# Optimization experiments

Measured on AMD Instinct MI355X. Metric: run time of the kernel, lower is better.

## Reference

```python
import jax, jax.numpy as jnp
import numpy as np

EMB = 768
HEADS = 12
HEAD_DIM = EMB // HEADS  # 64
SCALE = HEAD_DIM ** -0.5


def setup_inputs() -> dict:
    key = jax.random.key(0)
    ks = jax.random.split(key, 9)
    B, S = 32, 576
    s = EMB ** -0.5
    return {
        "hidden_states": jax.random.normal(ks[0], (B, S, EMB), jnp.float32),
        "q_w": jax.random.normal(ks[1], (EMB, EMB), jnp.float32) * s,
        "q_b": jnp.zeros((EMB,), jnp.float32),
        "k_w": jax.random.normal(ks[2], (EMB, EMB), jnp.float32) * s,
        "k_b": jnp.zeros((EMB,), jnp.float32),
        "v_w": jax.random.normal(ks[3], (EMB, EMB), jnp.float32) * s,
        "v_b": jnp.zeros((EMB,), jnp.float32),
        "o_w": jax.random.normal(ks[4], (EMB, EMB), jnp.float32) * s,
        "o_b": jnp.zeros((EMB,), jnp.float32),
    }


def reference(hidden_states, q_w, q_b, k_w, k_b, v_w, v_b, o_w, o_b):
    B, S, _ = hidden_states.shape
    # Linear projections (torch Linear: x @ W^T + b)
    q = hidden_states @ q_w.T + q_b
    k = hidden_states @ k_w.T + k_b
    v = hidden_states @ v_w.T + v_b
    # [B, H, S, D]
    q = q.reshape(B, S, HEADS, HEAD_DIM).transpose(0, 2, 1, 3)
    k = k.reshape(B, S, HEADS, HEAD_DIM).transpose(0, 2, 1, 3)
    v = v.reshape(B, S, HEADS, HEAD_DIM).transpose(0, 2, 1, 3)
    # Full N x N attention scores, softmax in fp32 (as in source)
    scores = jnp.einsum('bhqd,bhkd->bhqk', q, k) * SCALE
    attn = jax.nn.softmax(scores.astype(jnp.float32), axis=-1).astype(q.dtype)
    # dropout p=0.0 -> identity
    out = jnp.einsum('bhqk,bhkd->bhqd', attn, v)  # [B, H, S, D]
    out = out.transpose(0, 2, 1, 3).reshape(B, S, EMB)
    out = out @ o_w.T + o_b
    return (out, attn)
```

## Files before the change

### kernel.cpp

```cpp
#include <hip/hip_runtime.h>


#define B_ 32
#define S_ 576
#define H_ 12
#define D_ 64
#define E_ 768
#define M_ (B_ * S_)

typedef __attribute__((ext_vector_type(8))) short bf16x8;
typedef __attribute__((ext_vector_type(4))) float f32x4;
typedef __attribute__((ext_vector_type(4))) unsigned short u16x4;
typedef __attribute__((ext_vector_type(8))) unsigned short u16x8;

#define MFMA16(a, b, c) __builtin_amdgcn_mfma_f32_16x16x32_bf16(a, b, c, 0, 0, 0)

__device__ __forceinline__ unsigned short f2bf(float x) {
  union { float f; unsigned u; } v; v.f = x;
  unsigned r = v.u + 0x7fffu + ((v.u >> 16) & 1u);
  return (unsigned short)(r >> 16);
}
__device__ __forceinline__ float bf2f(unsigned short h) {
  union { unsigned u; float f; } v; v.u = ((unsigned)h) << 16; return v.f;
}

__global__ __launch_bounds__(256) void cvt_split(const float* __restrict__ in,
                                                 unsigned short* __restrict__ hi,
                                                 unsigned short* __restrict__ lo,
                                                 int n4) {
  int i = blockIdx.x * 256 + threadIdx.x;
  if (i >= n4) return;
  float4 x = ((const float4*)in)[i];
  u16x4 h;
  h[0] = f2bf(x.x); h[1] = f2bf(x.y); h[2] = f2bf(x.z); h[3] = f2bf(x.w);
  ((u16x4*)hi)[i] = h;
  if (lo) {
    u16x4 l;
    l[0] = f2bf(x.x - bf2f(h[0])); l[1] = f2bf(x.y - bf2f(h[1]));
    l[2] = f2bf(x.z - bf2f(h[2])); l[3] = f2bf(x.w - bf2f(h[3]));
    ((u16x4*)lo)[i] = l;
  }
}

template <bool SPLIT, int OUT_MODE>
__global__ __launch_bounds__(256)
void gemm128(const unsigned short* __restrict__ Ahg, const unsigned short* __restrict__ Alg,
             const unsigned short* __restrict__ Bhg, const unsigned short* __restrict__ Blg,
             const float* __restrict__ bias, void* __restrict__ C0, void* __restrict__ C1,
             int Kd, int lda, int ldb, int ldc) {
  constexpr int BM = 128, BN = 128, BK = 32, LSTR = BK + 8;
  __shared__ __attribute__((aligned(16))) unsigned short Ah[BM * LSTR];
  __shared__ __attribute__((aligned(16))) unsigned short Bh[BN * LSTR];
  __shared__ __attribute__((aligned(16))) unsigned short Al[SPLIT ? BM * LSTR : 8];
  __shared__ __attribute__((aligned(16))) unsigned short Bl[SPLIT ? BN * LSTR : 8];

  const int tid = threadIdx.x, lane = tid & 63, wv = tid >> 6;
  const int wm = (wv & 1) * 64, wn = (wv >> 1) * 64;
  const long m0 = (long)blockIdx.y * BM, n0 = (long)blockIdx.x * BN;
  const int fr = lane & 15, g8 = (lane >> 4) * 8;

  f32x4 acc[4][4] = {};

  for (int kt = 0; kt < Kd; kt += BK) {
    __syncthreads();
    for (int i = tid; i < BM * BK / 8; i += 256) {
      int row = i >> 2, c8 = (i & 3) * 8;
      *(u16x8*)&Ah[row * LSTR + c8] = *(const u16x8*)(Ahg + (m0 + row) * lda + kt + c8);
      *(u16x8*)&Bh[row * LSTR + c8] = *(const u16x8*)(Bhg + (n0 + row) * ldb + kt + c8);
      if (SPLIT) {
        *(u16x8*)&Al[row * LSTR + c8] = *(const u16x8*)(Alg + (m0 + row) * lda + kt + c8);
        *(u16x8*)&Bl[row * LSTR + c8] = *(const u16x8*)(Blg + (n0 + row) * ldb + kt + c8);
      }
    }
    __syncthreads();
    bf16x8 ah[4], bh[4], al[4], bl[4];
#pragma unroll
    for (int mi = 0; mi < 4; ++mi) {
      ah[mi] = *(const bf16x8*)&Ah[(wm + mi * 16 + fr) * LSTR + g8];
      if (SPLIT) al[mi] = *(const bf16x8*)&Al[(wm + mi * 16 + fr) * LSTR + g8];
    }
#pragma unroll
    for (int ni = 0; ni < 4; ++ni) {
      bh[ni] = *(const bf16x8*)&Bh[(wn + ni * 16 + fr) * LSTR + g8];
      if (SPLIT) bl[ni] = *(const bf16x8*)&Bl[(wn + ni * 16 + fr) * LSTR + g8];
    }
#pragma unroll
    for (int mi = 0; mi < 4; ++mi)
#pragma unroll
      for (int ni = 0; ni < 4; ++ni) {
        acc[mi][ni] = MFMA16(ah[mi], bh[ni], acc[mi][ni]);
        if (SPLIT) {
          acc[mi][ni] = MFMA16(ah[mi], bl[ni], acc[mi][ni]);
          acc[mi][ni] = MFMA16(al[mi], bh[ni], acc[mi][ni]);
        }
      }
  }

#pragma unroll
  for (int mi = 0; mi < 4; ++mi)
#pragma unroll
    for (int ni = 0; ni < 4; ++ni) {
      long col = n0 + wn + ni * 16 + fr;
      long rb = m0 + wm + mi * 16 + (lane >> 4) * 4;
      float bv = bias ? bias[col] : 0.f;
#pragma unroll
      for (int r = 0; r < 4; ++r) {
        float v = acc[mi][ni][r] + bv;
        long idx = (rb + r) * ldc + col;
        if (OUT_MODE == 0) {
          ((float*)C0)[idx] = v;
        } else if (OUT_MODE == 1) {
          ((unsigned short*)C0)[idx] = f2bf(v);
        } else {
          unsigned short hh = f2bf(v);
          ((unsigned short*)C0)[idx] = hh;
          ((unsigned short*)C1)[idx] = f2bf(v - bf2f(hh));
        }
      }
    }
}

__global__ __launch_bounds__(256)
void attn_softmax(const unsigned short* __restrict__ qh, const unsigned short* __restrict__ ql,
                  const unsigned short* __restrict__ kh, const unsigned short* __restrict__ kl,
                  float* __restrict__ attn) {
  constexpr int LQ = 72;
  __shared__ __attribute__((aligned(16))) unsigned short qhl[32 * LQ], qll[32 * LQ];
  __shared__ __attribute__((aligned(16))) unsigned short khl[64 * LQ], kll[64 * LQ];
  __shared__ float redm[2][32], reds[2][32];

  const int tid = threadIdx.x, lane = tid & 63, wv = tid >> 6;
  const int qt = blockIdx.x, h = blockIdx.y, b = blockIdx.z;
  const int fr = lane & 15, gq = lane >> 4;
  const int mg = (wv & 1), ch = (wv >> 1);

  {
    int row = tid >> 3, c8 = (tid & 7) * 8;
    long qb = ((long)(b * S_ + qt * 32 + row)) * E_ + h * 64 + c8;
    *(u16x8*)&qhl[row * LQ + c8] = *(const u16x8*)(qh + qb);
    *(u16x8*)&qll[row * LQ + c8] = *(const u16x8*)(ql + qb);
  }
  __syncthreads();
  bf16x8 qa_h[2], qa_l[2];
#pragma unroll
  for (int kc = 0; kc < 2; ++kc) {
    qa_h[kc] = *(const bf16x8*)&qhl[(mg * 16 + fr) * LQ + kc * 32 + gq * 8];
    qa_l[kc] = *(const bf16x8*)&qll[(mg * 16 + fr) * LQ + kc * 32 + gq * 8];
  }

  f32x4 acc[9][2] = {};
  for (int kt = 0; kt < 9; ++kt) {
    __syncthreads();
    for (int i = tid; i < 512; i += 256) {
      int row = i >> 3, c8 = (i & 7) * 8;
      long kb = ((long)(b * S_ + kt * 64 + row)) * E_ + h * 64 + c8;
      *(u16x8*)&khl[row * LQ + c8] = *(const u16x8*)(kh + kb);
      *(u16x8*)&kll[row * LQ + c8] = *(const u16x8*)(kl + kb);
    }
    __syncthreads();
#pragma unroll
    for (int kc = 0; kc < 2; ++kc) {
#pragma unroll
      for (int nf = 0; nf < 2; ++nf) {
        bf16x8 b_h = *(const bf16x8*)&khl[(ch * 32 + nf * 16 + fr) * LQ + kc * 32 + gq * 8];
        bf16x8 b_l = *(const bf16x8*)&kll[(ch * 32 + nf * 16 + fr) * LQ + kc * 32 + gq * 8];
        acc[kt][nf] = MFMA16(qa_h[kc], b_h, acc[kt][nf]);
        acc[kt][nf] = MFMA16(qa_h[kc], b_l, acc[kt][nf]);
        acc[kt][nf] = MFMA16(qa_l[kc], b_h, acc[kt][nf]);
      }
    }
  }

  const float SC = 0.125f;
  float M[4], Sv[4];
#pragma unroll
  for (int r = 0; r < 4; ++r) {
    float pm = -1e30f;
#pragma unroll
    for (int kt = 0; kt < 9; ++kt)
#pragma unroll
      for (int nf = 0; nf < 2; ++nf) pm = fmaxf(pm, acc[kt][nf][r] * SC);
    for (int off = 1; off < 16; off <<= 1) pm = fmaxf(pm, __shfl_xor(pm, off));
    M[r] = pm;
  }
  if (fr == 0) {
#pragma unroll
    for (int r = 0; r < 4; ++r) redm[ch][mg * 16 + gq * 4 + r] = M[r];
  }
  __syncthreads();
#pragma unroll
  for (int r = 0; r < 4; ++r)
    M[r] = fmaxf(redm[0][mg * 16 + gq * 4 + r], redm[1][mg * 16 + gq * 4 + r]);

#pragma unroll
  for (int r = 0; r < 4; ++r) {
    float ps = 0.f;
#pragma unroll
    for (int kt = 0; kt < 9; ++kt)
#pragma unroll
      for (int nf = 0; nf < 2; ++nf) {
        float e = __expf(acc[kt][nf][r] * SC - M[r]);
        acc[kt][nf][r] = e;
        ps += e;
      }
    for (int off = 1; off < 16; off <<= 1) ps += __shfl_xor(ps, off);
    Sv[r] = ps;
  }
  if (fr == 0) {
#pragma unroll
    for (int r = 0; r < 4; ++r) reds[ch][mg * 16 + gq * 4 + r] = Sv[r];
  }
  __syncthreads();
#pragma unroll
  for (int r = 0; r < 4; ++r)
    Sv[r] = 1.f / (reds[0][mg * 16 + gq * 4 + r] + reds[1][mg * 16 + gq * 4 + r]);

  float* out = attn + ((long)((b * H_ + h) * S_) + qt * 32) * S_;
#pragma unroll
  for (int kt = 0; kt < 9; ++kt)
#pragma unroll
    for (int nf = 0; nf < 2; ++nf)
#pragma unroll
      for (int r = 0; r < 4; ++r) {
        long row = mg * 16 + gq * 4 + r;
        long col = kt * 64 + ch * 32 + nf * 16 + fr;
        out[row * S_ + col] = acc[kt][nf][r] * Sv[r];
      }
}

__global__ __launch_bounds__(256)
void pv_kernel(const float* __restrict__ attn, const unsigned short* __restrict__ v,
               unsigned short* __restrict__ out_pre) {
  constexpr int LSTR = 40;
  __shared__ __attribute__((aligned(16))) unsigned short A_lds[64 * LSTR];
  __shared__ __attribute__((aligned(16))) unsigned short B_lds[64 * LSTR];

  const int tid = threadIdx.x, lane = tid & 63, wv = tid >> 6;
  const int mt = blockIdx.x, z = blockIdx.y;
  const int b = z / 12, h = z % 12;
  const int wm = (wv & 1) * 32, wn = (wv >> 1) * 32;
  const int fr = lane & 15, g8 = (lane >> 4) * 8;

  const float* Ab = attn + (long)z * S_ * S_ + (long)mt * 64 * S_;
  const unsigned short* Vb = v + (long)b * S_ * E_ + h * 64;

  f32x4 acc[2][2] = {};
  for (int kt = 0; kt < S_; kt += 32) {
    __syncthreads();
    for (int i = tid; i < 512; i += 256) {
      int row = i >> 3, c4 = (i & 7) * 4;
      float4 x = *(const float4*)(Ab + (long)row * S_ + kt + c4);
      u16x4 hh;
      hh[0] = f2bf(x.x); hh[1] = f2bf(x.y); hh[2] = f2bf(x.z); hh[3] = f2bf(x.w);
      *(u16x4*)&A_lds[row * LSTR + c4] = hh;
    }
    for (int i = tid; i < 512; i += 256) {
      int kk = i >> 4, d4 = (i & 15) * 4;
      u16x4 x = *(const u16x4*)(Vb + (long)(kt + kk) * E_ + d4);
#pragma unroll
      for (int j = 0; j < 4; ++j) B_lds[(d4 + j) * LSTR + kk] = x[j];
    }
    __syncthreads();
    bf16x8 af[2], bfv[2];
#pragma unroll
    for (int mi = 0; mi < 2; ++mi) af[mi] = *(const bf16x8*)&A_lds[(wm + mi * 16 + fr) * LSTR + g8];
#pragma unroll
    for (int ni = 0; ni < 2; ++ni) bfv[ni] = *(const bf16x8*)&B_lds[(wn + ni * 16 + fr) * LSTR + g8];
#pragma unroll
    for (int mi = 0; mi < 2; ++mi)
#pragma unroll
      for (int ni = 0; ni < 2; ++ni) acc[mi][ni] = MFMA16(af[mi], bfv[ni], acc[mi][ni]);
  }

#pragma unroll
  for (int mi = 0; mi < 2; ++mi)
#pragma unroll
    for (int ni = 0; ni < 2; ++ni)
#pragma unroll
      for (int r = 0; r < 4; ++r) {
        long row = (long)mt * 64 + wm + mi * 16 + (lane >> 4) * 4 + r;
        long col = wn + ni * 16 + fr;
        out_pre[((long)b * S_ + row) * E_ + h * 64 + col] = f2bf(acc[mi][ni][r]);
      }
}

extern "C" void kernel_launch(void* const* d_in, const int* in_sizes, int n_in,
                              void* d_out, int out_size, void* d_ws, size_t ws_size,
                              hipStream_t stream) {
  const float* X = (const float*)d_in[0];
  const float* q_w = (const float*)d_in[1];
  const float* q_b = (const float*)d_in[2];
  const float* k_w = (const float*)d_in[3];
  const float* k_b = (const float*)d_in[4];
  const float* v_w = (const float*)d_in[5];
  const float* v_b = (const float*)d_in[6];
  const float* o_w = (const float*)d_in[7];
  const float* o_b = (const float*)d_in[8];

  const long NX = (long)M_ * E_;
  const long NW = (long)E_ * E_;

  unsigned short* w = (unsigned short*)d_ws;
  unsigned short* Xhi = w;
  unsigned short* Xlo = Xhi + NX;
  unsigned short* qwh = Xlo + NX;
  unsigned short* qwl = qwh + NW;
  unsigned short* kwh = qwl + NW;
  unsigned short* kwl = kwh + NW;
  unsigned short* vwh = kwl + NW;
  unsigned short* owh = vwh + NW;
  unsigned short* Qhi = owh + NW;
  unsigned short* Qlo = Qhi + NX;
  unsigned short* Khi = Qlo + NX;
  unsigned short* Klo = Khi + NX;
  unsigned short* Vw  = Klo + NX;
  unsigned short* Opre = Vw + NX;

  float* out_f = (float*)d_out;
  float* attn_f = (float*)d_out + NX;

  cvt_split<<<dim3((NX / 4 + 255) / 256), dim3(256), 0, stream>>>(X, Xhi, Xlo, NX / 4);
  cvt_split<<<dim3((NW / 4 + 255) / 256), dim3(256), 0, stream>>>(q_w, qwh, qwl, NW / 4);
  cvt_split<<<dim3((NW / 4 + 255) / 256), dim3(256), 0, stream>>>(k_w, kwh, kwl, NW / 4);
  cvt_split<<<dim3((NW / 4 + 255) / 256), dim3(256), 0, stream>>>(v_w, vwh, nullptr, NW / 4);
  cvt_split<<<dim3((NW / 4 + 255) / 256), dim3(256), 0, stream>>>(o_w, owh, nullptr, NW / 4);

  dim3 gproj(E_ / 128, M_ / 128);
  gemm128<true, 2><<<gproj, dim3(256), 0, stream>>>(Xhi, Xlo, qwh, qwl, q_b, Qhi, Qlo, E_, E_, E_, E_);
  gemm128<true, 2><<<gproj, dim3(256), 0, stream>>>(Xhi, Xlo, kwh, kwl, k_b, Khi, Klo, E_, E_, E_, E_);
  gemm128<false, 1><<<gproj, dim3(256), 0, stream>>>(Xhi, nullptr, vwh, nullptr, v_b, Vw, nullptr, E_, E_, E_, E_);

  attn_softmax<<<dim3(S_ / 32, H_, B_), dim3(256), 0, stream>>>(Qhi, Qlo, Khi, Klo, attn_f);

  pv_kernel<<<dim3(S_ / 64, B_ * H_), dim3(256), 0, stream>>>(attn_f, Vw, Opre);

  gemm128<false, 0><<<gproj, dim3(256), 0, stream>>>(Opre, nullptr, owh, nullptr, o_b, out_f, nullptr, E_, E_, E_, E_);
}
```

Measured before the change: 1.216 ms.

## Fuse PV matmul into attention-softmax kernel with transposed V layout

Merges the separate PV kernel into the softmax kernel. The normalized probabilities are kept as bf16 in LDS and multiplied by V directly, so the fp32 attention matrix no longer has to be re-read from global memory. The V projection GEMM now writes V transposed per head ([B,H,D,S]) so V tiles load contiguously, and the attention output uses nontemporal stores. This adds a large P buffer in LDS (about 37KB), which may reduce occupancy, and the transposed V write is a strided scatter.

Measured after the change: 1.197 ms. No clear change (-1.6%).

```diff
diff --git a/kernel.cpp b/kernel.cpp
--- a/kernel.cpp
+++ b/kernel.cpp
@@ -111,23 +111,33 @@
           ((float*)C0)[idx] = v;
         } else if (OUT_MODE == 1) {
           ((unsigned short*)C0)[idx] = f2bf(v);
-        } else {
+        } else if (OUT_MODE == 2) {
           unsigned short hh = f2bf(v);
           ((unsigned short*)C0)[idx] = hh;
           ((unsigned short*)C1)[idx] = f2bf(v - bf2f(hh));
+        } else {
+          long m = rb + r;
+          int bb = (int)(m / S_);
+          int ss = (int)(m - (long)bb * S_);
+          int hh2 = (int)(col >> 6), dd = (int)(col & 63);
+          ((unsigned short*)C0)[(((long)bb * H_ + hh2) * D_ + dd) * S_ + ss] = f2bf(v);
         }
       }
     }
 }
 
 __global__ __launch_bounds__(256)
-void attn_softmax(const unsigned short* __restrict__ qh, const unsigned short* __restrict__ ql,
-                  const unsigned short* __restrict__ kh, const unsigned short* __restrict__ kl,
-                  float* __restrict__ attn) {
+void attn_pv(const unsigned short* __restrict__ qh, const unsigned short* __restrict__ ql,
+             const unsigned short* __restrict__ kh, const unsigned short* __restrict__ kl,
+             const unsigned short* __restrict__ vt,
+             float* __restrict__ attn, unsigned short* __restrict__ out_pre) {
   constexpr int LQ = 72;
+  constexpr int LP = 584;
   __shared__ __attribute__((aligned(16))) unsigned short qhl[32 * LQ], qll[32 * LQ];
   __shared__ __attribute__((aligned(16))) unsigned short khl[64 * LQ], kll[64 * LQ];
+  __shared__ __attribute__((aligned(16))) unsigned short P_lds[32 * LP];
   __shared__ float redm[2][32], reds[2][32];
+  unsigned short* Vt = kll;
 
   const int tid = threadIdx.x, lane = tid & 63, wv = tid >> 6;
   const int qt = blockIdx.x, h = blockIdx.y, b = blockIdx.z;
@@ -222,66 +232,41 @@
     for (int nf = 0; nf < 2; ++nf)
 #pragma unroll
       for (int r = 0; r < 4; ++r) {
-        long row = mg * 16 + gq * 4 + r;
-        long col = kt * 64 + ch * 32 + nf * 16 + fr;
-        out[row * S_ + col] = acc[kt][nf][r] * Sv[r];
-      }
-}
-
-__global__ __launch_bounds__(256)
-void pv_kernel(const float* __restrict__ attn, const unsigned short* __restrict__ v,
-               unsigned short* __restrict__ out_pre) {
-  constexpr int LSTR = 40;
-  __shared__ __attribute__((aligned(16))) unsigned short A_lds[64 * LSTR];
-  __shared__ __attribute__((aligned(16))) unsigned short B_lds[64 * LSTR];
-
-  const int tid = threadIdx.x, lane = tid & 63, wv = tid >> 6;
-  const int mt = blockIdx.x, z = blockIdx.y;
-  const int b = z / 12, h = z % 12;
-  const int wm = (wv & 1) * 32, wn = (wv >> 1) * 32;
-  const int fr = lane & 15, g8 = (lane >> 4) * 8;
-
-  const float* Ab = attn + (long)z * S_ * S_ + (long)mt * 64 * S_;
-  const unsigned short* Vb = v + (long)b * S_ * E_ + h * 64;
-
-  f32x4 acc[2][2] = {};
-  for (int kt = 0; kt < S_; kt += 32) {
+        int row = mg * 16 + gq * 4 + r;
+        int col = kt * 64 + ch * 32 + nf * 16 + fr;
+        float val = acc[kt][nf][r] * Sv[r];
+        __builtin_nontemporal_store(val, &out[(long)row * S_ + col]);
+        P_lds[row * LP + col] = f2bf(val);
+      }
+
+  const unsigned short* Vb = vt + ((long)(b * H_ + h)) * D_ * S_;
+  f32x4 accp[2] = {};
+  for (int kt2 = 0; kt2 < 9; ++kt2) {
     __syncthreads();
     for (int i = tid; i < 512; i += 256) {
-      int row = i >> 3, c4 = (i & 7) * 4;
-      float4 x = *(const float4*)(Ab + (long)row * S_ + kt + c4);
-      u16x4 hh;
-      hh[0] = f2bf(x.x); hh[1] = f2bf(x.y); hh[2] = f2bf(x.z); hh[3] = f2bf(x.w);
-      *(u16x4*)&A_lds[row * LSTR + c4] = hh;
-    }
-    for (int i = tid; i < 512; i += 256) {
-      int kk = i >> 4, d4 = (i & 15) * 4;
-      u16x4 x = *(const u16x4*)(Vb + (long)(kt + kk) * E_ + d4);
-#pragma unroll
-      for (int j = 0; j < 4; ++j) B_lds[(d4 + j) * LSTR + kk] = x[j];
-    }
-    __syncthreads();
-    bf16x8 af[2], bfv[2];
-#pragma unroll
-    for (int mi = 0; mi < 2; ++mi) af[mi] = *(const bf16x8*)&A_lds[(wm + mi * 16 + fr) * LSTR + g8];
-#pragma unroll
-    for (int ni = 0; ni < 2; ++ni) bfv[ni] = *(const bf16x8*)&B_lds[(wn + ni * 16 + fr) * LSTR + g8];
-#pragma unroll
-    for (int mi = 0; mi < 2; ++mi)
-#pragma unroll
-      for (int ni = 0; ni < 2; ++ni) acc[mi][ni] = MFMA16(af[mi], bfv[ni], acc[mi][ni]);
-  }
-
-#pragma unroll
-  for (int mi = 0; mi < 2; ++mi)
-#pragma unroll
-    for (int ni = 0; ni < 2; ++ni)
-#pragma unroll
-      for (int r = 0; r < 4; ++r) {
-        long row = (long)mt * 64 + wm + mi * 16 + (lane >> 4) * 4 + r;
-        long col = wn + ni * 16 + fr;
-        out_pre[((long)b * S_ + row) * E_ + h * 64 + col] = f2bf(acc[mi][ni][r]);
-      }
+      int row = i >> 3, c8 = (i & 7) * 8;
+      *(u16x8*)&Vt[row * LQ + c8] = *(const u16x8*)(Vb + (long)row * S_ + kt2 * 64 + c8);
+    }
+    __syncthreads();
+#pragma unroll
+    for (int kc = 0; kc < 2; ++kc) {
+      bf16x8 a = *(const bf16x8*)&P_lds[(mg * 16 + fr) * LP + kt2 * 64 + kc * 32 + gq * 8];
+#pragma unroll
+      for (int ni = 0; ni < 2; ++ni) {
+        bf16x8 bv = *(const bf16x8*)&Vt[(ch * 32 + ni * 16 + fr) * LQ + kc * 32 + gq * 8];
+        accp[ni] = MFMA16(a, bv, accp[ni]);
+      }
+    }
+  }
+
+#pragma unroll
+  for (int ni = 0; ni < 2; ++ni)
+#pragma unroll
+    for (int r = 0; r < 4; ++r) {
+      int row = mg * 16 + gq * 4 + r;
+      int col = ch * 32 + ni * 16 + fr;
+      out_pre[((long)b * S_ + qt * 32 + row) * E_ + h * 64 + col] = f2bf(accp[ni][r]);
+    }
 }
 
 extern "C" void kernel_launch(void* const* d_in, const int* in_sizes, int n_in,
@@ -313,8 +298,8 @@
   unsigned short* Qlo = Qhi + NX;
   unsigned short* Khi = Qlo + NX;
   unsigned short* Klo = Khi + NX;
-  unsigned short* Vw  = Klo + NX;
-  unsigned short* Opre = Vw + NX;
+  unsigned short* Vt  = Klo + NX;
+  unsigned short* Opre = Vt + NX;
 
   float* out_f = (float*)d_out;
   float* attn_f = (float*)d_out + NX;
@@ -328,11 +313,9 @@
   dim3 gproj(E_ / 128, M_ / 128);
   gemm128<true, 2><<<gproj, dim3(256), 0, stream>>>(Xhi, Xlo, qwh, qwl, q_b, Qhi, Qlo, E_, E_, E_, E_);
   gemm128<true, 2><<<gproj, dim3(256), 0, stream>>>(Xhi, Xlo, kwh, kwl, k_b, Khi, Klo, E_, E_, E_, E_);
-  gemm128<false, 1><<<gproj, dim3(256), 0, stream>>>(Xhi, nullptr, vwh, nullptr, v_b, Vw, nullptr, E_, E_, E_, E_);
-
-  attn_softmax<<<dim3(S_ / 32, H_, B_), dim3(256), 0, stream>>>(Qhi, Qlo, Khi, Klo, attn_f);
-
-  pv_kernel<<<dim3(S_ / 64, B_ * H_), dim3(256), 0, stream>>>(attn_f, Vw, Opre);
+  gemm128<false, 3><<<gproj, dim3(256), 0, stream>>>(Xhi, nullptr, vwh, nullptr, v_b, Vt, nullptr, E_, E_, E_, E_);
+
+  attn_pv<<<dim3(S_ / 32, H_, B_), dim3(256), 0, stream>>>(Qhi, Qlo, Khi, Klo, Vt, attn_f, Opre);
 
   gemm128<false, 0><<<gproj, dim3(256), 0, stream>>>(Opre, nullptr, owh, nullptr, o_b, out_f, nullptr, E_, E_, E_, E_);
 }
```
